# Kernel tuning notes

Hardware: AMD Instinct MI355X
Metric: run time of the kernel (lower is better)

## Reference

```python
import jax, jax.numpy as jnp
import numpy as np

N_STATE = 1024
N_HEAD = 16
D_K = N_STATE // N_HEAD  # 64


def setup_inputs() -> dict:
    key = jax.random.key(0)
    ks = jax.random.split(key, 12)
    B, S = 2, 2048
    s = 1.0 / np.sqrt(N_STATE)
    inp = {
        "q": jax.random.normal(ks[0], (B, S, N_STATE), jnp.float32),
        "k": jax.random.normal(ks[1], (B, S, N_STATE), jnp.float32),
        "v": jax.random.normal(ks[2], (B, S, N_STATE), jnp.float32),
        # Linear weights in torch layout [out_features, in_features]
        "Wq": jax.random.normal(ks[3], (N_STATE, N_STATE), jnp.float32) * s,
        "bq": jax.random.normal(ks[4], (N_STATE,), jnp.float32) * s,
        "Wk": jax.random.normal(ks[5], (N_STATE, N_STATE), jnp.float32) * s,
        "bk": jax.random.normal(ks[6], (N_STATE,), jnp.float32) * s,
        "Wv": jax.random.normal(ks[7], (N_STATE, N_STATE), jnp.float32) * s,
        "bv": jax.random.normal(ks[8], (N_STATE,), jnp.float32) * s,
        "Wo": jax.random.normal(ks[9], (N_STATE, N_STATE), jnp.float32) * s,
        "bo": jax.random.normal(ks[10], (N_STATE,), jnp.float32) * s,
    }
    return inp


def reference(q, k, v, Wq, bq, Wk, bk, Wv, bv, Wo, bo):
    B = q.shape[0]
    # projections (torch Linear: x @ W.T + b), split heads -> [B, H, S, d]
    def proj(x, W, b):
        y = jnp.einsum('bsi,oi->bso', x, W) + b
        return y.reshape(B, -1, N_HEAD, D_K).transpose(0, 2, 1, 3)
    qh = proj(q, Wq, bq)
    kh = proj(k, Wk, bk)
    vh = proj(v, Wv, bv)
    # scaled dot-product attention, full [B,H,Sq,Sk] scores as in original
    scores = jnp.einsum('bhqd,bhkd->bhqk', qh, kh) / np.sqrt(D_K).astype(np.float32)
    attn = jax.nn.softmax(scores, axis=-1)
    out = jnp.einsum('bhqk,bhkd->bhqd', attn, vh)
    out = out.transpose(0, 2, 1, 3).reshape(B, -1, N_HEAD * D_K)
    return jnp.einsum('bsi,oi->bso', out, Wo) + bo
```

## Files before the change

kernel.cpp:

```cpp
#include <hip/hip_runtime.h>
#include <stdint.h>

typedef __attribute__((ext_vector_type(8))) short short8;
typedef __attribute__((ext_vector_type(4))) float f32x4;
typedef __attribute__((ext_vector_type(4))) uint32_t u32x4;

#if __has_builtin(__builtin_amdgcn_exp2f)
#define EXP2(x) __builtin_amdgcn_exp2f(x)
#else
#define EXP2(x) exp2f(x)
#endif

__device__ __forceinline__ short f2bf(float f){
  uint32_t u = __builtin_bit_cast(uint32_t, f);
  return (short)((u + 0x8000u) >> 16);
}
__device__ __forceinline__ uint32_t pk2(float lo, float hi){
  uint32_t a = __builtin_bit_cast(uint32_t, lo) + 0x8000u;
  uint32_t b = __builtin_bit_cast(uint32_t, hi) + 0x8000u;
#if __has_builtin(__builtin_amdgcn_perm)
  return __builtin_amdgcn_perm(b, a, 0x07060302u);
#else
  return (b & 0xFFFF0000u) | (a >> 16);
#endif
}
__device__ __forceinline__ void gload16(const void* g, void* l){
  __builtin_amdgcn_global_load_lds((const __attribute__((address_space(1))) void*)g,
                                   (__attribute__((address_space(3))) void*)l, 16, 0, 0);
}

__global__ __launch_bounds__(512) void cvt_all(
    const float* __restrict__ q, const float* __restrict__ k, const float* __restrict__ v,
    const float* __restrict__ wq, const float* __restrict__ wk, const float* __restrict__ wv,
    const float* __restrict__ wo, short* __restrict__ dst){
  const size_t SQ = 4096ull*1024ull, NW = 1024ull*1024ull;
  size_t e = (size_t)(blockIdx.x*512u + threadIdx.x)*8ull;
  const float* src; size_t rel;
  if (e < 3*SQ){ size_t which = e / SQ; src = which==0?q:(which==1?k:v); rel = e - which*SQ; }
  else { size_t e2 = e - 3*SQ; size_t which = e2 / NW;
         src = which==0?wq:(which==1?wk:(which==2?wv:wo)); rel = e2 - which*NW; }
  float4 a = *(const float4*)(src + rel);
  float4 b = *(const float4*)(src + rel + 4);
  u32x4 r = { pk2(a.x,a.y), pk2(a.z,a.w), pk2(b.x,b.y), pk2(b.z,b.w) };
  *(u32x4*)(dst + e) = r;
}

template<int MODE>
__device__ __forceinline__ void gemm_body(const short* __restrict__ A, const short* __restrict__ Bw,
    const float* __restrict__ bias, void* __restrict__ Cout, float scale, int m0, int n0){
  const int K = 1024;
  __shared__ short Al[128*64];
  __shared__ short Bl[128*64];
  int tid = threadIdx.x;
  int w = tid >> 6, lane = tid & 63, lr = lane & 15, lg = lane >> 4;
  int wr = w >> 2, wc = w & 3;
  f32x4 acc[4][2] = {};
  int row0 = tid >> 3;
  int qc0  = (tid & 7) ^ (row0 & 7);
  const short* Ag = A  + (size_t)(m0 + row0)*K + qc0*8;
  const short* Bg = Bw + (size_t)(n0 + row0)*K + qc0*8;
  char* Alb = (char*)Al + tid*16;
  char* Blb = (char*)Bl + tid*16;
  int ra[4], rb[2];
#pragma unroll
  for (int mi=0; mi<4; ++mi) ra[mi] = wr*64 + mi*16 + lr;
#pragma unroll
  for (int ni=0; ni<2; ++ni) rb[ni] = wc*32 + ni*16 + lr;
  for (int k0 = 0; k0 < K; k0 += 64){
    gload16(Ag + k0,                Alb);
    gload16(Ag + k0 + 64*(size_t)K, Alb + 8192);
    gload16(Bg + k0,                Blb);
    gload16(Bg + k0 + 64*(size_t)K, Blb + 8192);
    __syncthreads();
#pragma unroll
    for (int kk=0; kk<2; ++kk){
      short8 av[4], bv[2];
#pragma unroll
      for (int mi=0; mi<4; ++mi)
        av[mi] = *(const short8*)((char*)Al + ra[mi]*128 + (((kk*4 + lg) ^ (ra[mi] & 7)) << 4));
#pragma unroll
      for (int ni=0; ni<2; ++ni)
        bv[ni] = *(const short8*)((char*)Bl + rb[ni]*128 + (((kk*4 + lg) ^ (rb[ni] & 7)) << 4));
#pragma unroll
      for (int mi=0; mi<4; ++mi)
#pragma unroll
        for (int ni=0; ni<2; ++ni){
          if (MODE == 2)
            acc[mi][ni] = __builtin_amdgcn_mfma_f32_16x16x32_bf16(bv[ni], av[mi], acc[mi][ni], 0, 0, 0);
          else
            acc[mi][ni] = __builtin_amdgcn_mfma_f32_16x16x32_bf16(av[mi], bv[ni], acc[mi][ni], 0, 0, 0);
        }
    }
    __syncthreads();
  }
#pragma unroll
  for (int ni=0; ni<2; ++ni){
#pragma unroll
    for (int mi=0; mi<4; ++mi){
      if (MODE == 2){
        int srow = m0 + wr*64 + mi*16 + lr;
        int b = srow >> 11, s = srow & 2047;
#pragma unroll
        for (int i2=0; i2<4; ++i2){
          int dcol = n0 + wc*32 + ni*16 + lg*4 + i2;
          int h = dcol >> 6, d = dcol & 63;
          float val = acc[mi][ni][i2] + bias[dcol];
          ((short*)Cout)[(((size_t)(b*16 + h))*64 + d)*2048 + s] = f2bf(val);
        }
      } else {
        int col = n0 + wc*32 + ni*16 + lr;
        float bb = bias[col];
#pragma unroll
        for (int i2=0; i2<4; ++i2){
          int row = m0 + wr*64 + mi*16 + lg*4 + i2;
          float val = (acc[mi][ni][i2] + bb) * scale;
          if (MODE == 0){
            int b = row >> 11, s = row & 2047, h = col >> 6, d = col & 63;
            ((short*)Cout)[(((size_t)(b*16 + h))*2048 + s)*64 + d] = f2bf(val);
          } else {
            ((float*)Cout)[(size_t)row*1024 + col] = val;
          }
        }
      }
    }
  }
}

__global__ __launch_bounds__(512) void gemm_qkv(
    const short* __restrict__ qb, const short* __restrict__ kb, const short* __restrict__ vb,
    const short* __restrict__ Wqb, const short* __restrict__ Wkb, const short* __restrict__ Wvb,
    const float* __restrict__ bq, const float* __restrict__ bk, const float* __restrict__ bv,
    short* __restrict__ Qh, short* __restrict__ Kh, short* __restrict__ VhT, float qscale){
  int f = blockIdx.y*gridDim.x + blockIdx.x;
  int L = (f & 7)*96 + (f >> 3);
  int z = L >> 8, r = L & 255;
  int m0 = (r >> 3)*128, n0 = (r & 7)*128;
  const short* A  = z==0 ? qb  : (z==1 ? kb  : vb);
  const short* Bw = z==0 ? Wqb : (z==1 ? Wkb : Wvb);
  const float* bi = z==0 ? bq  : (z==1 ? bk  : bv);
  short* C        = z==0 ? Qh  : (z==1 ? Kh  : VhT);
  if (z == 2) gemm_body<2>(A, Bw, bi, (void*)C, 1.0f, m0, n0);
  else        gemm_body<0>(A, Bw, bi, (void*)C, z==0 ? qscale : 1.0f, m0, n0);
}

__global__ __launch_bounds__(512) void gemm_out(const short* __restrict__ A, const short* __restrict__ Bw,
    const float* __restrict__ bias, float* __restrict__ Cout){
  int f = blockIdx.y*gridDim.x + blockIdx.x;
  int L = (f & 7)*32 + (f >> 3);
  int m0 = (L >> 3)*128, n0 = (L & 7)*128;
  gemm_body<1>(A, Bw, bias, (void*)Cout, 1.0f, m0, n0);
}

__global__ __launch_bounds__(512) void attn_fwd(const short* __restrict__ Qh, const short* __restrict__ Kh,
    const short* __restrict__ VhT, short* __restrict__ AO){
  const int S = 2048;
  int i = blockIdx.y*gridDim.x + blockIdx.x;
  int L = (i & 7)*64 + (i >> 3);
  int bh = L >> 4, qt = L & 15;
  __shared__ short Kl[4][4096];
  __shared__ short Vl[4][4096];
  int tid = threadIdx.x, w = tid >> 6, lane = tid & 63, lr = lane & 15, lg = lane >> 4;
  const short* Qb = Qh  + (size_t)bh*S*64;
  const short* Kb = Kh  + (size_t)bh*S*64;
  const short* Vb = VhT + (size_t)bh*64*2048;
  int q0 = qt*128 + w*16;
  short8 aq[2];
#pragma unroll
  for (int h=0; h<2; ++h)
    aq[h] = *(const short8*)&Qb[(size_t)(q0 + lr)*64 + h*32 + lg*8];
  f32x4 o[4] = {};
  f32x4 o1 = {};
  short8 ones;
#pragma unroll
  for (int j=0; j<8; ++j) ones[j] = (short)0x3F80;
  int koff = tid*16;
  int kr = tid >> 3, kc = tid & 7;
  int ksw = (kr & 3) | (((kr >> 3) & 1) << 2);
  int ksrc = kr*64 + ((kc ^ ksw) << 3);
  int vsrc = kr*2048 + ((kc ^ (kr & 7)) << 3);
  int Rbase = 8*(lr >> 2) + (lr & 3);
  int sR = (lr & 3) | (((lr >> 2) & 1) << 2);
  int slot0 = (lg ^ sR) << 3, slot1 = ((lg + 4) ^ sR) << 3;
  int vx = lr & 7;
#pragma unroll
  for (int t=0; t<4; ++t){
    gload16(Kb + (size_t)t*4096 + ksrc, (char*)&Kl[t][0] + koff);
    gload16(Vb + vsrc + t*64,           (char*)&Vl[t][0] + koff);
  }
  asm volatile("s_waitcnt vmcnt(4)" ::: "memory");
  __builtin_amdgcn_sched_barrier(0);
  __builtin_amdgcn_s_barrier();

  for (int p = 0; p < 16; ++p){
    short8 pa[2][2];
    __builtin_amdgcn_s_setprio(1);
#pragma unroll
    for (int u = 0; u < 2; ++u){
      const short* Kbuf = &Kl[(2*p + u) & 3][0];
      uint32_t Wp[2][2][2];
#pragma unroll
      for (int nf=0; nf<4; ++nf){
        int R = Rbase + (nf & 1)*4 + (nf >> 1)*32;
        short8 ak0 = *(const short8*)&Kbuf[R*64 + slot0];
        short8 ak1 = *(const short8*)&Kbuf[R*64 + slot1];
        f32x4 z = {};
        z = __builtin_amdgcn_mfma_f32_16x16x32_bf16(ak0, aq[0], z, 0, 0, 0);
        z = __builtin_amdgcn_mfma_f32_16x16x32_bf16(ak1, aq[1], z, 0, 0, 0);
        float p0 = EXP2(z[0]), p1 = EXP2(z[1]);
        float p2 = EXP2(z[2]), p3 = EXP2(z[3]);
        Wp[nf >> 1][nf & 1][0] = pk2(p0, p1);
        Wp[nf >> 1][nf & 1][1] = pk2(p2, p3);
      }
#pragma unroll
      for (int c=0; c<2; ++c){
        union { uint32_t u4[4]; short8 s; } tt;
        tt.u4[0] = Wp[c][0][0]; tt.u4[1] = Wp[c][0][1];
        tt.u4[2] = Wp[c][1][0]; tt.u4[3] = Wp[c][1][1];
        pa[u][c] = tt.s;
      }
    }
#pragma unroll
    for (int u = 0; u < 2; ++u){
      const short* Vbuf = &Vl[(2*p + u) & 3][0];
#pragma unroll
      for (int df=0; df<4; ++df){
        int rowv = (df*16 + lr)*64;
        short8 vb0 = *(const short8*)&Vbuf[rowv + ((lg ^ vx) << 3)];
        short8 vb1 = *(const short8*)&Vbuf[rowv + (((4 + lg) ^ vx) << 3)];
        o[df] = __builtin_amdgcn_mfma_f32_16x16x32_bf16(pa[u][0], vb0, o[df], 0, 0, 0);
        o[df] = __builtin_amdgcn_mfma_f32_16x16x32_bf16(pa[u][1], vb1, o[df], 0, 0, 0);
      }
      o1 = __builtin_amdgcn_mfma_f32_16x16x32_bf16(pa[u][0], ones, o1, 0, 0, 0);
      o1 = __builtin_amdgcn_mfma_f32_16x16x32_bf16(pa[u][1], ones, o1, 0, 0, 0);
    }
    __builtin_amdgcn_s_setprio(0);
    if (p < 15){
      asm volatile("s_waitcnt vmcnt(0)" ::: "memory");
      __builtin_amdgcn_sched_barrier(0);
      __builtin_amdgcn_s_barrier();
      if (p < 14){
#pragma unroll
        for (int u = 0; u < 2; ++u){
          int t = 2*p + 4 + u, nb = t & 3;
          gload16(Kb + (size_t)t*4096 + ksrc, (char*)&Kl[nb][0] + koff);
          gload16(Vb + vsrc + t*64,           (char*)&Vl[nb][0] + koff);
        }
      }
    }
  }
  int b = bh >> 4, hh = bh & 15;
  float rinv[4];
#pragma unroll
  for (int i2=0; i2<4; ++i2) rinv[i2] = 1.0f / o1[i2];
#pragma unroll
  for (int df=0; df<4; ++df)
#pragma unroll
    for (int i2=0; i2<4; ++i2){
      int row = q0 + lg*4 + i2;
      int col = df*16 + lr;
      AO[((size_t)(b*2048 + row))*1024 + hh*64 + col] = f2bf(o[df][i2] * rinv[i2]);
    }
}

extern "C" void kernel_launch(void* const* d_in, const int* in_sizes, int n_in,
                              void* d_out, int out_size, void* d_ws, size_t ws_size,
                              hipStream_t stream){
  const float* q  = (const float*)d_in[0];
  const float* k  = (const float*)d_in[1];
  const float* v  = (const float*)d_in[2];
  const float* Wq = (const float*)d_in[3];
  const float* bq = (const float*)d_in[4];
  const float* Wk = (const float*)d_in[5];
  const float* bk = (const float*)d_in[6];
  const float* Wv = (const float*)d_in[7];
  const float* bv = (const float*)d_in[8];
  const float* Wo = (const float*)d_in[9];
  const float* bo = (const float*)d_in[10];

  const size_t SQ = 4096ull*1024ull, NW = 1024ull*1024ull;
  short* ws  = (short*)d_ws;
  short* qb  = ws;
  short* kb  = ws + SQ;
  short* vb  = ws + 2*SQ;
  short* Wqb = ws + 3*SQ;
  short* Wkb = Wqb + NW;
  short* Wvb = Wkb + NW;
  short* Wob = Wvb + NW;
  short* Qh  = Wob + NW;
  short* Kh  = Qh + SQ;
  short* VhT = Kh + SQ;
  short* AO  = qb;

  const float Csc = 0.18033688011112042f;

  cvt_all<<<4096, 512, 0, stream>>>(q, k, v, Wq, Wk, Wv, Wo, ws);
  gemm_qkv<<<dim3(16, 48), 512, 0, stream>>>(qb, kb, vb, Wqb, Wkb, Wvb, bq, bk, bv, Qh, Kh, VhT, Csc);
  attn_fwd<<<dim3(16, 32), 512, 0, stream>>>(Qh, Kh, VhT, AO);
  gemm_out<<<dim3(16, 16), 512, 0, stream>>>(AO, Wob, bo, (float*)d_out);
}
```

Baseline: 115.0 us.

## Double-buffer LDS tiles in projection GEMM to overlap loads with MFMA

Splits the GEMM's shared-memory A and B tiles into two buffers and prefetches the next K-slice with direct global-to-LDS loads while MFMAs run on the current one. The two barriers per K step become a single wait-plus-barrier at the top of each iteration. This aims to hide global load latency inside the projection GEMMs. The cost is double the LDS use per block (64KB), which may reduce occupancy.

```diff
diff --git a/kernel.cpp b/kernel.cpp
--- a/kernel.cpp
+++ b/kernel.cpp
@@ -49,8 +49,8 @@
 __device__ __forceinline__ void gemm_body(const short* __restrict__ A, const short* __restrict__ Bw,
     const float* __restrict__ bias, void* __restrict__ Cout, float scale, int m0, int n0){
   const int K = 1024;
-  __shared__ short Al[128*64];
-  __shared__ short Bl[128*64];
+  __shared__ short Al[2][128*64];
+  __shared__ short Bl[2][128*64];
   int tid = threadIdx.x;
   int w = tid >> 6, lane = tid & 63, lr = lane & 15, lg = lane >> 4;
   int wr = w >> 2, wc = w & 3;
@@ -59,28 +59,44 @@
   int qc0  = (tid & 7) ^ (row0 & 7);
   const short* Ag = A  + (size_t)(m0 + row0)*K + qc0*8;
   const short* Bg = Bw + (size_t)(n0 + row0)*K + qc0*8;
-  char* Alb = (char*)Al + tid*16;
-  char* Blb = (char*)Bl + tid*16;
   int ra[4], rb[2];
 #pragma unroll
   for (int mi=0; mi<4; ++mi) ra[mi] = wr*64 + mi*16 + lr;
 #pragma unroll
   for (int ni=0; ni<2; ++ni) rb[ni] = wc*32 + ni*16 + lr;
-  for (int k0 = 0; k0 < K; k0 += 64){
-    gload16(Ag + k0,                Alb);
-    gload16(Ag + k0 + 64*(size_t)K, Alb + 8192);
-    gload16(Bg + k0,                Blb);
-    gload16(Bg + k0 + 64*(size_t)K, Blb + 8192);
-    __syncthreads();
+  {
+    char* Ad = (char*)&Al[0][0] + tid*16;
+    char* Bd = (char*)&Bl[0][0] + tid*16;
+    gload16(Ag,                Ad);
+    gload16(Ag + 64*(size_t)K, Ad + 8192);
+    gload16(Bg,                Bd);
+    gload16(Bg + 64*(size_t)K, Bd + 8192);
+  }
+  for (int it = 0; it < 16; ++it){
+    int buf = it & 1;
+    asm volatile("s_waitcnt vmcnt(0)" ::: "memory");
+    __builtin_amdgcn_sched_barrier(0);
+    __builtin_amdgcn_s_barrier();
+    if (it < 15){
+      int k1 = (it + 1)*64;
+      char* Ad = (char*)&Al[buf^1][0] + tid*16;
+      char* Bd = (char*)&Bl[buf^1][0] + tid*16;
+      gload16(Ag + k1,                Ad);
+      gload16(Ag + k1 + 64*(size_t)K, Ad + 8192);
+      gload16(Bg + k1,                Bd);
+      gload16(Bg + k1 + 64*(size_t)K, Bd + 8192);
+    }
+    const char* Ab = (const char*)&Al[buf][0];
+    const char* Bb = (const char*)&Bl[buf][0];
 #pragma unroll
     for (int kk=0; kk<2; ++kk){
       short8 av[4], bv[2];
 #pragma unroll
       for (int mi=0; mi<4; ++mi)
-        av[mi] = *(const short8*)((char*)Al + ra[mi]*128 + (((kk*4 + lg) ^ (ra[mi] & 7)) << 4));
+        av[mi] = *(const short8*)(Ab + ra[mi]*128 + (((kk*4 + lg) ^ (ra[mi] & 7)) << 4));
 #pragma unroll
       for (int ni=0; ni<2; ++ni)
-        bv[ni] = *(const short8*)((char*)Bl + rb[ni]*128 + (((kk*4 + lg) ^ (rb[ni] & 7)) << 4));
+        bv[ni] = *(const short8*)(Bb + rb[ni]*128 + (((kk*4 + lg) ^ (rb[ni] & 7)) << 4));
 #pragma unroll
       for (int mi=0; mi<4; ++mi)
 #pragma unroll
@@ -91,7 +107,6 @@
             acc[mi][ni] = __builtin_amdgcn_mfma_f32_16x16x32_bf16(av[mi], bv[ni], acc[mi][ni], 0, 0, 0);
         }
     }
-    __syncthreads();
   }
 #pragma unroll
   for (int ni=0; ni<2; ++ni){
```

Measured after the change: 121.5 us. +5.7%, slower.

## Load V tiles directly from global into registers instead of staging through LDS

Applied to the files above, without the earlier changes.

Removes the shared-memory V buffers and their async global-to-LDS prefetch. Each wave now reads its V^T fragments straight from global memory into registers at the start of every key tile, and only K stays double-buffered in LDS. This halves LDS usage and drops the V LDS reads, which may allow more resident blocks. The cost is that all eight waves in a block load the same V tile redundantly through the caches, and the global load latency now sits inside the loop, only partly hidden behind the QK^T MFMAs and exp work.

```diff
diff --git a/kernel.cpp b/kernel.cpp
--- a/kernel.cpp
+++ b/kernel.cpp
@@ -158,7 +158,6 @@
   int L = (i & 7)*64 + (i >> 3);
   int bh = L >> 4, qt = L & 15;
   __shared__ short Kl[4][4096];
-  __shared__ short Vl[4][4096];
   int tid = threadIdx.x, w = tid >> 6, lane = tid & 63, lr = lane & 15, lg = lane >> 4;
   const short* Qb = Qh  + (size_t)bh*S*64;
   const short* Kb = Kh  + (size_t)bh*S*64;
@@ -177,61 +176,63 @@
   int kr = tid >> 3, kc = tid & 7;
   int ksw = (kr & 3) | (((kr >> 3) & 1) << 2);
   int ksrc = kr*64 + ((kc ^ ksw) << 3);
-  int vsrc = kr*2048 + ((kc ^ (kr & 7)) << 3);
   int Rbase = 8*(lr >> 2) + (lr & 3);
   int sR = (lr & 3) | (((lr >> 2) & 1) << 2);
   int slot0 = (lg ^ sR) << 3, slot1 = ((lg + 4) ^ sR) << 3;
-  int vx = lr & 7;
-#pragma unroll
-  for (int t=0; t<4; ++t){
+  int vrow[4];
+#pragma unroll
+  for (int df=0; df<4; ++df) vrow[df] = (df*16 + lr)*2048 + lg*8;
+#pragma unroll
+  for (int t=0; t<4; ++t)
     gload16(Kb + (size_t)t*4096 + ksrc, (char*)&Kl[t][0] + koff);
-    gload16(Vb + vsrc + t*64,           (char*)&Vl[t][0] + koff);
-  }
-  asm volatile("s_waitcnt vmcnt(4)" ::: "memory");
+  asm volatile("s_waitcnt vmcnt(2)" ::: "memory");
   __builtin_amdgcn_sched_barrier(0);
   __builtin_amdgcn_s_barrier();
 
   for (int p = 0; p < 16; ++p){
-    short8 pa[2][2];
     __builtin_amdgcn_s_setprio(1);
 #pragma unroll
     for (int u = 0; u < 2; ++u){
-      const short* Kbuf = &Kl[(2*p + u) & 3][0];
-      uint32_t Wp[2][2][2];
-#pragma unroll
-      for (int nf=0; nf<4; ++nf){
-        int R = Rbase + (nf & 1)*4 + (nf >> 1)*32;
-        short8 ak0 = *(const short8*)&Kbuf[R*64 + slot0];
-        short8 ak1 = *(const short8*)&Kbuf[R*64 + slot1];
-        f32x4 z = {};
-        z = __builtin_amdgcn_mfma_f32_16x16x32_bf16(ak0, aq[0], z, 0, 0, 0);
-        z = __builtin_amdgcn_mfma_f32_16x16x32_bf16(ak1, aq[1], z, 0, 0, 0);
-        float p0 = EXP2(z[0]), p1 = EXP2(z[1]);
-        float p2 = EXP2(z[2]), p3 = EXP2(z[3]);
-        Wp[nf >> 1][nf & 1][0] = pk2(p0, p1);
-        Wp[nf >> 1][nf & 1][1] = pk2(p2, p3);
-      }
-#pragma unroll
-      for (int c=0; c<2; ++c){
-        union { uint32_t u4[4]; short8 s; } tt;
-        tt.u4[0] = Wp[c][0][0]; tt.u4[1] = Wp[c][0][1];
-        tt.u4[2] = Wp[c][1][0]; tt.u4[3] = Wp[c][1][1];
-        pa[u][c] = tt.s;
-      }
-    }
-#pragma unroll
-    for (int u = 0; u < 2; ++u){
-      const short* Vbuf = &Vl[(2*p + u) & 3][0];
+      int t = 2*p + u;
+      short8 vf[4][2];
+      int tcol = t*64;
 #pragma unroll
       for (int df=0; df<4; ++df){
-        int rowv = (df*16 + lr)*64;
-        short8 vb0 = *(const short8*)&Vbuf[rowv + ((lg ^ vx) << 3)];
-        short8 vb1 = *(const short8*)&Vbuf[rowv + (((4 + lg) ^ vx) << 3)];
-        o[df] = __builtin_amdgcn_mfma_f32_16x16x32_bf16(pa[u][0], vb0, o[df], 0, 0, 0);
-        o[df] = __builtin_amdgcn_mfma_f32_16x16x32_bf16(pa[u][1], vb1, o[df], 0, 0, 0);
-      }
-      o1 = __builtin_amdgcn_mfma_f32_16x16x32_bf16(pa[u][0], ones, o1, 0, 0, 0);
-      o1 = __builtin_amdgcn_mfma_f32_16x16x32_bf16(pa[u][1], ones, o1, 0, 0, 0);
+        vf[df][0] = *(const short8*)&Vb[vrow[df] + tcol];
+        vf[df][1] = *(const short8*)&Vb[vrow[df] + tcol + 32];
+      }
+      const short* Kbuf = &Kl[t & 3][0];
+      short8 pa[2];
+      {
+        uint32_t Wp[2][2][2];
+#pragma unroll
+        for (int nf=0; nf<4; ++nf){
+          int R = Rbase + (nf & 1)*4 + (nf >> 1)*32;
+          short8 ak0 = *(const short8*)&Kbuf[R*64 + slot0];
+          short8 ak1 = *(const short8*)&Kbuf[R*64 + slot1];
+          f32x4 z = {};
+          z = __builtin_amdgcn_mfma_f32_16x16x32_bf16(ak0, aq[0], z, 0, 0, 0);
+          z = __builtin_amdgcn_mfma_f32_16x16x32_bf16(ak1, aq[1], z, 0, 0, 0);
+          float p0 = EXP2(z[0]), p1 = EXP2(z[1]);
+          float p2 = EXP2(z[2]), p3 = EXP2(z[3]);
+          Wp[nf >> 1][nf & 1][0] = pk2(p0, p1);
+          Wp[nf >> 1][nf & 1][1] = pk2(p2, p3);
+        }
+#pragma unroll
+        for (int c=0; c<2; ++c){
+          union { uint32_t u4[4]; short8 s; } tt;
+          tt.u4[0] = Wp[c][0][0]; tt.u4[1] = Wp[c][0][1];
+          tt.u4[2] = Wp[c][1][0]; tt.u4[3] = Wp[c][1][1];
+          pa[c] = tt.s;
+        }
+      }
+#pragma unroll
+      for (int df=0; df<4; ++df){
+        o[df] = __builtin_amdgcn_mfma_f32_16x16x32_bf16(pa[0], vf[df][0], o[df], 0, 0, 0);
+        o[df] = __builtin_amdgcn_mfma_f32_16x16x32_bf16(pa[1], vf[df][1], o[df], 0, 0, 0);
+      }
+      o1 = __builtin_amdgcn_mfma_f32_16x16x32_bf16(pa[0], ones, o1, 0, 0, 0);
+      o1 = __builtin_amdgcn_mfma_f32_16x16x32_bf16(pa[1], ones, o1, 0, 0, 0);
     }
     __builtin_amdgcn_s_setprio(0);
     if (p < 15){
@@ -241,9 +242,8 @@
       if (p < 14){
 #pragma unroll
         for (int u = 0; u < 2; ++u){
-          int t = 2*p + 4 + u, nb = t & 3;
-          gload16(Kb + (size_t)t*4096 + ksrc, (char*)&Kl[nb][0] + koff);
-          gload16(Vb + vsrc + t*64,           (char*)&Vl[nb][0] + koff);
+          int t = 2*p + 4 + u;
+          gload16(Kb + (size_t)t*4096 + ksrc, (char*)&Kl[t & 3][0] + koff);
         }
       }
     }
```

After: 191.2 us. +66.3%, slower.
